# Optimization experiments

Hardware: AMD Instinct MI355X
Metric: run time of the kernel (lower is better)

## Reference

```python
import jax, jax.numpy as jnp
import numpy as np
import math

EPS = 1e-12
ANCHOR_T = 2.91  # anchor ratio threshold
G = 0.5          # grid-cell offset bias
OFF = np.array([[0, 0], [1, 0], [0, 1], [-1, 0], [0, -1]], dtype=np.float32) * G


def _bce_with_logits(x, t, pos_weight):
    # mean of -[pw*t*log(sig(x)) + (1-t)*log(1-sig(x))], numerically stable
    return jnp.mean((1.0 - t) * x + (1.0 + (pos_weight - 1.0) * t) * jax.nn.softplus(-x))


def _bbox_ciou(box1, box2):
    # box1, box2: [M,4] in xywh format (matches bbox_iou(x1y1x2y2=False, CIoU=True))
    b1_x1 = box1[:, 0] - box1[:, 2] / 2
    b1_x2 = box1[:, 0] + box1[:, 2] / 2 + EPS
    b1_y1 = box1[:, 1] - box1[:, 3] / 2
    b1_y2 = box1[:, 1] + box1[:, 3] / 2 + EPS
    b2_x1 = box2[:, 0] - box2[:, 2] / 2
    b2_x2 = box2[:, 0] + box2[:, 2] / 2 + EPS
    b2_y1 = box2[:, 1] - box2[:, 3] / 2
    b2_y2 = box2[:, 1] + box2[:, 3] / 2 + EPS
    inter = (jnp.clip(jnp.minimum(b1_x2, b2_x2) - jnp.maximum(b1_x1, b2_x1), 0)
             * jnp.clip(jnp.minimum(b1_y2, b2_y2) - jnp.maximum(b1_y1, b2_y1), 0))
    w1, h1 = b1_x2 - b1_x1, b1_y2 - b1_y1
    w2, h2 = b2_x2 - b2_x1, b2_y2 - b2_y1
    union = w1 * h1 + w2 * h2 - inter
    iou = inter / union
    cw = jnp.maximum(b1_x2, b2_x2) - jnp.minimum(b1_x1, b2_x1)
    ch = jnp.maximum(b1_y2, b2_y2) - jnp.minimum(b1_y1, b2_y1)
    c2 = cw ** 2 + ch ** 2
    rho2 = ((b2_x1 + b2_x2 - (b1_x1 + b1_x2)) ** 2 / 4
            + (b2_y1 + b2_y2 - (b1_y1 + b1_y2)) ** 2 / 4)
    v = (4.0 / math.pi ** 2) * (jnp.arctan(w2 / h2) - jnp.arctan(w1 / h1)) ** 2
    alpha = jax.lax.stop_gradient(v / (1.0 + EPS - iou + v))
    return iou - (rho2 / c2 + v * alpha)


def build_targets(p_shapes, targets, anchors):
    # Eager (non-jit) target assignment; returns per-level (tcls, tbox, indices, anch)
    na = anchors.shape[1]
    nl = anchors.shape[0]
    nt = targets.shape[0]
    ai = jnp.tile(jnp.arange(na, dtype=targets.dtype)[:, None], (1, nt))
    t7 = jnp.concatenate([jnp.tile(targets[None], (na, 1, 1)), ai[:, :, None]], axis=2)  # [na,nt,7]
    off = jnp.asarray(OFF)
    out = []
    for i in range(nl):
        anc = anchors[i]  # [na,2] in grid units
        W, H = p_shapes[i][3], p_shapes[i][2]
        gain = jnp.array([1, 1, W, H, W, H, 1], dtype=targets.dtype)
        t = t7 * gain
        r = t[:, :, 4:6] / anc[:, None, :]
        jmask = jnp.max(jnp.maximum(r, 1.0 / r), axis=2) < ANCHOR_T  # [na,nt]
        t = t[jmask]  # [M,7]
        gxy = t[:, 2:4]
        gxi = jnp.array([W, H], dtype=t.dtype) - gxy
        jk = (gxy % 1.0 < G) & (gxy > 1.0)
        lm = (gxi % 1.0 < G) & (gxi > 1.0)
        m5 = jnp.stack([jnp.ones_like(jk[:, 0]), jk[:, 0], jk[:, 1], lm[:, 0], lm[:, 1]])  # [5,M]
        t5 = jnp.tile(t[None], (5, 1, 1))[m5]
        offs = (jnp.zeros_like(gxy)[None] + off[:, None, :])[m5]
        b = t5[:, 0].astype(jnp.int32)
        c = t5[:, 1].astype(jnp.int32)
        gxy = t5[:, 2:4]
        gwh = t5[:, 4:6]
        gij = (gxy - offs).astype(jnp.int32)  # trunc == floor for positive coords
        gi, gj = gij[:, 0], gij[:, 1]
        a = t5[:, 6].astype(jnp.int32)
        tbox = jnp.concatenate([gxy - gij.astype(gxy.dtype), gwh], axis=1)
        out.append((c, tbox, (b, a, gj, gi), anc[a]))
    return out


def loss_from_built(p_list, built, num_classes):
    h_cls_pw, h_obj_pw = 0.631, 0.911
    h_giou, h_obj, h_cls = 0.0296, 0.301, 0.243
    balance = [4.0, 1.0, 0.4]
    lbox = jnp.zeros((), p_list[0].dtype)
    lobj = jnp.zeros((), p_list[0].dtype)
    lcls = jnp.zeros((), p_list[0].dtype)
    for i, pi in enumerate(p_list):
        tcls_i, tbox_i, (b, a, gj, gi), anch_i = built[i]
        tobj = jnp.zeros(pi.shape[:4], pi.dtype)
        n = b.shape[0]
        if n:
            ps = pi[b, a, gj, gi]  # [n, 5+nc]
            pxy = jax.nn.sigmoid(ps[:, :2]) * 2.0 - 0.5
            pwh = (jax.nn.sigmoid(ps[:, 2:4]) * 2.0) ** 2 * anch_i
            pbox = jnp.concatenate([pxy, pwh], axis=1)
            ciou = _bbox_ciou(pbox, tbox_i)
            lbox = lbox + jnp.mean(1.0 - ciou)
            tobj = tobj.at[b, a, gj, gi].set(
                jax.lax.stop_gradient(jnp.clip(ciou, 0.0, None)).astype(tobj.dtype))
            if num_classes > 1:
                tcl = jnp.zeros((n, num_classes), pi.dtype).at[jnp.arange(n), tcls_i].set(1.0)
                lcls = lcls + _bce_with_logits(ps[:, 5:], tcl, h_cls_pw)
        lobj = lobj + _bce_with_logits(pi[..., 4], tobj, h_obj_pw) * balance[i]
    s = 3.0 / len(p_list)
    lbox = lbox * h_giou * s
    lobj = lobj * h_obj * s
    lcls = lcls * h_cls * s
    loss = lbox + lobj + lcls
    bs = p_list[0].shape[0]
    return loss * bs, jnp.stack([lbox, lobj, lcls, loss])


def setup_inputs() -> dict:
    key = jax.random.key(0)
    k0, k1, k2, k3, k4, k5, k6 = jax.random.split(key, 7)
    B, nc, nt = 16, 80, 400
    p0 = jax.random.normal(k0, (B, 3, 80, 80, 5 + nc), jnp.float32)
    p1 = jax.random.normal(k1, (B, 3, 40, 40, 5 + nc), jnp.float32)
    p2 = jax.random.normal(k2, (B, 3, 20, 20, 5 + nc), jnp.float32)
    img = jax.random.randint(k3, (nt, 1), 0, B).astype(jnp.float32)
    cls = jax.random.randint(k4, (nt, 1), 0, nc).astype(jnp.float32)
    xy = jax.random.uniform(k5, (nt, 2), jnp.float32, 0.05, 0.95)
    wh = jax.random.uniform(k6, (nt, 2), jnp.float32, 0.02, 0.30)
    targets = jnp.concatenate([img, cls, xy, wh], axis=1)  # [nt,6]
    anchors = jnp.array([  # COCO yolov5 anchors / stride, [nl, na, 2]
        [[1.25, 1.625], [2.0, 3.75], [4.125, 2.875]],
        [[1.875, 3.8125], [3.875, 2.8125], [3.6875, 7.4375]],
        [[3.625, 2.8125], [4.875, 6.1875], [11.65625, 10.1875]]], dtype=jnp.float32)
    return {"p0": p0, "p1": p1, "p2": p2, "targets": targets, "anchors": anchors}


def reference(p0, p1, p2, targets, anchors):
    p_list = [p0, p1, p2]
    built = build_targets([p.shape for p in p_list], targets, anchors)
    return loss_from_built(p_list, built, num_classes=80)
```

## Files before the change

### kernel.cpp

```cpp
#include <hip/hip_runtime.h>
#include <math.h>

namespace {

constexpr int kMaxNT = 1024;
constexpr int kCells0 = 16 * 3 * 80 * 80;
constexpr int kCells1 = 16 * 3 * 40 * 40;
constexpr int kCells2 = 16 * 3 * 20 * 20;
constexpr int kCellsTotal = kCells0 + kCells1 + kCells2;

constexpr int kSlotsPerBlock = 16;
constexpr int kObjBlocks = 256;
constexpr int kObjThreads = kObjBlocks * 256;
constexpr int kObjIters = (kCellsTotal + kObjThreads - 1) / kObjThreads;

constexpr int kBPLMax = (15 * kMaxNT + kSlotsPerBlock - 1) / kSlotsPerBlock;

constexpr size_t kEbOff    = 0;
constexpr size_t kOpartOff = kEbOff + 4 * (3 * kBPLMax);

__device__ __forceinline__ float softplus_neg(float x) {
  return fmaxf(-x, 0.0f) + log1pf(expf(-fabsf(x)));
}

__global__ __launch_bounds__(256) void main_kernel(
    const float* __restrict__ p0, const float* __restrict__ p1,
    const float* __restrict__ p2, const float* __restrict__ targets,
    const float* __restrict__ anchors,
    float* __restrict__ eb_lbox, float* __restrict__ eb_lcls,
    float* __restrict__ eb_cnt, float* __restrict__ eb_ocorr,
    float* __restrict__ opart, int nt, int bpl) {
  int bid = blockIdx.x;
  int tid = threadIdx.x;
  int group = tid >> 6;
  int lane = tid & 63;

  if (bid < kObjBlocks) {
    int flat0 = bid * 256 + tid;
    float x[kObjIters];
#pragma unroll
    for (int j = 0; j < kObjIters; ++j) {
      int cell = flat0 + j * kObjThreads;
      float v = 0.0f;
      if (cell < kCellsTotal) {
        const float* p;
        int rel;
        if (cell < kCells0) { p = p0; rel = cell; }
        else if (cell < kCells0 + kCells1) { p = p1; rel = cell - kCells0; }
        else { p = p2; rel = cell - kCells0 - kCells1; }
        v = __builtin_nontemporal_load(&p[(size_t)rel * 85 + 4]);
      }
      x[j] = v;
    }
    float a0 = 0.f, a1 = 0.f, a2 = 0.f;
#pragma unroll
    for (int j = 0; j < kObjIters; ++j) {
      int cell = flat0 + j * kObjThreads;
      if (cell < kCellsTotal) {
        float v = x[j] + softplus_neg(x[j]);
        if (cell < kCells0) a0 += v;
        else if (cell < kCells0 + kCells1) a1 += v;
        else a2 += v;
      }
    }
    for (int o = 32; o > 0; o >>= 1) {
      a0 += __shfl_xor(a0, o);
      a1 += __shfl_xor(a1, o);
      a2 += __shfl_xor(a2, o);
    }
    __shared__ float s0[4], s1[4], s2[4];
    if (lane == 0) { s0[group] = a0; s1[group] = a1; s2[group] = a2; }
    __syncthreads();
    if (tid == 0) {
      opart[bid * 3 + 0] = s0[0] + s0[1] + s0[2] + s0[3];
      opart[bid * 3 + 1] = s1[0] + s1[1] + s1[2] + s1[3];
      opart[bid * 3 + 2] = s2[0] + s2[1] + s2[2] + s2[3];
    }
    return;
  }

  int ebid = bid - kObjBlocks;
  int level = ebid / bpl;
  int blk = ebid - level * bpl;
  int nslots = 15 * nt;
  int Wi = (level == 0) ? 80 : (level == 1) ? 40 : 20;
  float W = (float)Wi;
  const float* p = (level == 0) ? p0 : (level == 1) ? p1 : p2;

  float lbox_acc = 0.0f, cnt_acc = 0.0f, cls_acc = 0.0f, oc_acc = 0.0f;

  for (int k = 0; k < 4; ++k) {
    int s = blk * kSlotsPerBlock + group * 4 + k;
    if (s >= nslots) break;
    int r = s % 5;
    int pair = s / 5;
    int a = pair / nt;
    int ti = pair - a * nt;
    const float* tg = targets + ti * 6;
    float gx = tg[2] * W, gy = tg[3] * W;
    float gw = tg[4] * W, gh = tg[5] * W;
    float aw = anchors[(level * 3 + a) * 2 + 0];
    float ah = anchors[(level * 3 + a) * 2 + 1];
    float rw = gw / aw, rh = gh / ah;
    float m = fmaxf(fmaxf(rw, 1.0f / rw), fmaxf(rh, 1.0f / rh));
    bool pass = m < 2.91f;

    bool rowok = true;
    float ox = 0.0f, oy = 0.0f;
    if (r == 1)      { rowok = (fmodf(gx, 1.0f) < 0.5f) && (gx > 1.0f); ox = 0.5f; }
    else if (r == 2) { rowok = (fmodf(gy, 1.0f) < 0.5f) && (gy > 1.0f); oy = 0.5f; }
    else if (r == 3) { float gxi = W - gx;
                       rowok = (fmodf(gxi, 1.0f) < 0.5f) && (gxi > 1.0f); ox = -0.5f; }
    else if (r == 4) { float gyi = W - gy;
                       rowok = (fmodf(gyi, 1.0f) < 0.5f) && (gyi > 1.0f); oy = -0.5f; }

    if (!(pass && rowok)) continue;

    int gi = min(max((int)(gx - ox), 0), Wi - 1);
    int gj = min(max((int)(gy - oy), 0), Wi - 1);
    int b = (int)tg[0];
    int cls = (int)tg[1];
    int cell = ((b * 3 + a) * Wi + gj) * Wi + gi;
    const float* ps = p + (size_t)cell * 85;
    float tbx = gx - (float)gi, tby = gy - (float)gj;

    float px = 2.0f / (1.0f + expf(-ps[0])) - 0.5f;
    float py = 2.0f / (1.0f + expf(-ps[1])) - 0.5f;
    float sw = 2.0f / (1.0f + expf(-ps[2]));
    float sh = 2.0f / (1.0f + expf(-ps[3]));
    float pw = sw * sw * aw;
    float ph = sh * sh * ah;

    const float EPS = 1e-12f;
    float b1x1 = px - pw * 0.5f, b1x2 = px + pw * 0.5f + EPS;
    float b1y1 = py - ph * 0.5f, b1y2 = py + ph * 0.5f + EPS;
    float b2x1 = tbx - gw * 0.5f, b2x2 = tbx + gw * 0.5f + EPS;
    float b2y1 = tby - gh * 0.5f, b2y2 = tby + gh * 0.5f + EPS;
    float iw = fminf(b1x2, b2x2) - fmaxf(b1x1, b2x1);
    float ih = fminf(b1y2, b2y2) - fmaxf(b1y1, b2y1);
    float inter = fmaxf(iw, 0.0f) * fmaxf(ih, 0.0f);
    float w1 = b1x2 - b1x1, h1 = b1y2 - b1y1;
    float w2 = b2x2 - b2x1, h2 = b2y2 - b2y1;
    float uni = w1 * h1 + w2 * h2 - inter;
    float iou = inter / uni;
    float cwd = fmaxf(b1x2, b2x2) - fminf(b1x1, b2x1);
    float chd = fmaxf(b1y2, b2y2) - fminf(b1y1, b2y1);
    float c2 = cwd * cwd + chd * chd;
    float dx = (b2x1 + b2x2) - (b1x1 + b1x2);
    float dy = (b2y1 + b2y2) - (b1y1 + b1y2);
    float rho2 = dx * dx * 0.25f + dy * dy * 0.25f;
    float dat = atanf(w2 / h2) - atanf(w1 / h1);
    float v = 0.4052847345693511f * dat * dat;
    float alpha = v / (1.0f + EPS - iou + v);
    float ciou = iou - (rho2 / c2 + v * alpha);

    {
      float x = ps[5 + lane];
      float sp = softplus_neg(x);
      cls_acc += (lane == cls) ? (0.631f * sp) : (x + sp);
    }
    if (lane < 16) {
      int c = lane + 64;
      float x = ps[5 + c];
      float sp = softplus_neg(x);
      cls_acc += (c == cls) ? (0.631f * sp) : (x + sp);
    }

    float t = fmaxf(ciou, 0.0f);
    float xo = ps[4];
    oc_acc += t * (-xo - 0.089f * softplus_neg(xo));

    lbox_acc += 1.0f - ciou;
    cnt_acc += 1.0f;
  }

  for (int o = 32; o > 0; o >>= 1) cls_acc += __shfl_xor(cls_acc, o);

  __shared__ float sb[4], sc[4], sn[4], so[4];
  if (lane == 0) {
    sb[group] = lbox_acc; sc[group] = cls_acc;
    sn[group] = cnt_acc;  so[group] = oc_acc;
  }
  __syncthreads();
  if (tid == 0) {
    eb_lbox[ebid]  = sb[0] + sb[1] + sb[2] + sb[3];
    eb_lcls[ebid]  = sc[0] + sc[1] + sc[2] + sc[3];
    eb_cnt[ebid]   = sn[0] + sn[1] + sn[2] + sn[3];
    eb_ocorr[ebid] = so[0] + so[1] + so[2] + so[3];
  }
}

__global__ __launch_bounds__(256) void final_kernel(
    const float* __restrict__ eb_lbox, const float* __restrict__ eb_lcls,
    const float* __restrict__ eb_cnt, const float* __restrict__ eb_ocorr,
    const float* __restrict__ opart, float* __restrict__ out, int bpl) {
  int tid = threadIdx.x;
  int lane = tid & 63, w = tid >> 6;

  double vals[12];
#pragma unroll
  for (int k = 0; k < 12; ++k) vals[k] = 0.0;

#pragma unroll
  for (int lvl = 0; lvl < 3; ++lvl) {
    for (int j = tid; j < bpl; j += 256) {
      int bi = lvl * bpl + j;
      vals[lvl]     += (double)eb_lbox[bi];
      vals[3 + lvl] += (double)eb_lcls[bi];
      vals[6 + lvl] += (double)eb_cnt[bi];
      vals[9 + lvl] += (double)eb_ocorr[bi];
    }
  }
  for (int j = tid; j < kObjBlocks; j += 256) {
    vals[9]  += (double)opart[j * 3 + 0];
    vals[10] += (double)opart[j * 3 + 1];
    vals[11] += (double)opart[j * 3 + 2];
  }

  __shared__ double red[4][12];
#pragma unroll
  for (int k = 0; k < 12; ++k) {
    double v = vals[k];
    for (int o = 32; o > 0; o >>= 1) v += __shfl_xor(v, o);
    if (lane == 0) red[w][k] = v;
  }
  __syncthreads();
  if (tid == 0) {
    const double bal[3] = {4.0, 1.0, 0.4};
    const double ncl[3] = {(double)kCells0, (double)kCells1, (double)kCells2};
    double lbox = 0.0, lcls = 0.0, lobj = 0.0;
#pragma unroll
    for (int l = 0; l < 3; ++l) {
      double sB = red[0][l] + red[1][l] + red[2][l] + red[3][l];
      double sC = red[0][3 + l] + red[1][3 + l] + red[2][3 + l] + red[3][3 + l];
      double n  = red[0][6 + l] + red[1][6 + l] + red[2][6 + l] + red[3][6 + l];
      double sO = red[0][9 + l] + red[1][9 + l] + red[2][9 + l] + red[3][9 + l];
      if (n > 0.0) {
        lbox += sB / n;
        lcls += sC / (n * 80.0);
      }
      lobj += sO / ncl[l] * bal[l];
    }
    lbox *= 0.0296;
    lobj *= 0.301;
    lcls *= 0.243;
    double loss = lbox + lobj + lcls;
    out[0] = (float)(loss * 16.0);
    out[1] = (float)lbox;
    out[2] = (float)lobj;
    out[3] = (float)lcls;
    out[4] = (float)loss;
  }
}

}

extern "C" void kernel_launch(void* const* d_in, const int* in_sizes, int n_in,
                              void* d_out, int out_size, void* d_ws, size_t ws_size,
                              hipStream_t stream) {
  const float* p0 = (const float*)d_in[0];
  const float* p1 = (const float*)d_in[1];
  const float* p2 = (const float*)d_in[2];
  const float* targets = (const float*)d_in[3];
  const float* anchors = (const float*)d_in[4];
  int nt = in_sizes[3] / 6;
  if (nt > kMaxNT) nt = kMaxNT;
  int nslots = 15 * nt;
  int bpl = (nslots + kSlotsPerBlock - 1) / kSlotsPerBlock;

  float* wsf = (float*)d_ws;
  float* eb_lbox = wsf + kEbOff;
  float* eb_lcls = eb_lbox + 3 * kBPLMax;
  float* eb_cnt = eb_lcls + 3 * kBPLMax;
  float* eb_ocorr = eb_cnt + 3 * kBPLMax;
  float* opart = wsf + kOpartOff;

  int gridA = kObjBlocks + 3 * bpl;
  main_kernel<<<gridA, 256, 0, stream>>>(p0, p1, p2, targets, anchors,
                                         eb_lbox, eb_lcls, eb_cnt, eb_ocorr,
                                         opart, nt, bpl);
  final_kernel<<<1, 256, 0, stream>>>(eb_lbox, eb_lcls, eb_cnt, eb_ocorr, opart,
                                      (float*)d_out, bpl);
}
```

Measured before the change: 31.56 us.

## Replace final reduction kernel with atomics and last-block finalize

Per-block partial sums now go straight into a 12-float global accumulator with float atomicAdd, and a completion counter lets the last block compute the final loss. This drops the separate final reduction kernel and its partial-sum arrays. A tiny arm kernel is launched first to zero the accumulator and counter, so the launch count stays at two. The final sums change from a double-precision tree reduction to float atomics, which adds contention on a few addresses and makes the rounding order nondeterministic.

```diff
diff --git a/kernel.cpp b/kernel.cpp
--- a/kernel.cpp
+++ b/kernel.cpp
@@ -14,26 +14,28 @@
 constexpr int kObjThreads = kObjBlocks * 256;
 constexpr int kObjIters = (kCellsTotal + kObjThreads - 1) / kObjThreads;
 
-constexpr int kBPLMax = (15 * kMaxNT + kSlotsPerBlock - 1) / kSlotsPerBlock;
-
-constexpr size_t kEbOff    = 0;
-constexpr size_t kOpartOff = kEbOff + 4 * (3 * kBPLMax);
-
 __device__ __forceinline__ float softplus_neg(float x) {
   return fmaxf(-x, 0.0f) + log1pf(expf(-fabsf(x)));
+}
+
+__global__ void arm_kernel(float* __restrict__ acc, int* __restrict__ counter) {
+  int t = threadIdx.x;
+  if (t < 12) acc[t] = 0.0f;
+  if (t == 12) *counter = 0;
 }
 
 __global__ __launch_bounds__(256) void main_kernel(
     const float* __restrict__ p0, const float* __restrict__ p1,
     const float* __restrict__ p2, const float* __restrict__ targets,
     const float* __restrict__ anchors,
-    float* __restrict__ eb_lbox, float* __restrict__ eb_lcls,
-    float* __restrict__ eb_cnt, float* __restrict__ eb_ocorr,
-    float* __restrict__ opart, int nt, int bpl) {
+    float* __restrict__ acc, int* __restrict__ counter,
+    float* __restrict__ out, int nt, int bpl) {
   int bid = blockIdx.x;
   int tid = threadIdx.x;
   int group = tid >> 6;
   int lane = tid & 63;
+
+  __shared__ float s0[4], s1[4], s2[4], s3[4];
 
   if (bid < kObjBlocks) {
     int flat0 = bid * 256 + tid;
@@ -68,162 +70,144 @@
       a1 += __shfl_xor(a1, o);
       a2 += __shfl_xor(a2, o);
     }
-    __shared__ float s0[4], s1[4], s2[4];
     if (lane == 0) { s0[group] = a0; s1[group] = a1; s2[group] = a2; }
     __syncthreads();
     if (tid == 0) {
-      opart[bid * 3 + 0] = s0[0] + s0[1] + s0[2] + s0[3];
-      opart[bid * 3 + 1] = s1[0] + s1[1] + s1[2] + s1[3];
-      opart[bid * 3 + 2] = s2[0] + s2[1] + s2[2] + s2[3];
-    }
-    return;
+      float t0 = s0[0] + s0[1] + s0[2] + s0[3];
+      float t1 = s1[0] + s1[1] + s1[2] + s1[3];
+      float t2 = s2[0] + s2[1] + s2[2] + s2[3];
+      atomicAdd(&acc[9], t0);
+      atomicAdd(&acc[10], t1);
+      atomicAdd(&acc[11], t2);
+    }
+  } else {
+    int ebid = bid - kObjBlocks;
+    int level = ebid / bpl;
+    int blk = ebid - level * bpl;
+    int nslots = 15 * nt;
+    int Wi = (level == 0) ? 80 : (level == 1) ? 40 : 20;
+    float W = (float)Wi;
+    const float* p = (level == 0) ? p0 : (level == 1) ? p1 : p2;
+
+    float lbox_acc = 0.0f, cnt_acc = 0.0f, cls_acc = 0.0f, oc_acc = 0.0f;
+
+    for (int k = 0; k < 4; ++k) {
+      int s = blk * kSlotsPerBlock + group * 4 + k;
+      if (s >= nslots) break;
+      int r = s % 5;
+      int pair = s / 5;
+      int a = pair / nt;
+      int ti = pair - a * nt;
+      const float* tg = targets + ti * 6;
+      float gx = tg[2] * W, gy = tg[3] * W;
+      float gw = tg[4] * W, gh = tg[5] * W;
+      float aw = anchors[(level * 3 + a) * 2 + 0];
+      float ah = anchors[(level * 3 + a) * 2 + 1];
+      float rw = gw / aw, rh = gh / ah;
+      float m = fmaxf(fmaxf(rw, 1.0f / rw), fmaxf(rh, 1.0f / rh));
+      bool pass = m < 2.91f;
+
+      bool rowok = true;
+      float ox = 0.0f, oy = 0.0f;
+      if (r == 1)      { rowok = (fmodf(gx, 1.0f) < 0.5f) && (gx > 1.0f); ox = 0.5f; }
+      else if (r == 2) { rowok = (fmodf(gy, 1.0f) < 0.5f) && (gy > 1.0f); oy = 0.5f; }
+      else if (r == 3) { float gxi = W - gx;
+                         rowok = (fmodf(gxi, 1.0f) < 0.5f) && (gxi > 1.0f); ox = -0.5f; }
+      else if (r == 4) { float gyi = W - gy;
+                         rowok = (fmodf(gyi, 1.0f) < 0.5f) && (gyi > 1.0f); oy = -0.5f; }
+
+      if (!(pass && rowok)) continue;
+
+      int gi = min(max((int)(gx - ox), 0), Wi - 1);
+      int gj = min(max((int)(gy - oy), 0), Wi - 1);
+      int b = (int)tg[0];
+      int cls = (int)tg[1];
+      int cell = ((b * 3 + a) * Wi + gj) * Wi + gi;
+      const float* ps = p + (size_t)cell * 85;
+      float tbx = gx - (float)gi, tby = gy - (float)gj;
+
+      float px = 2.0f / (1.0f + expf(-ps[0])) - 0.5f;
+      float py = 2.0f / (1.0f + expf(-ps[1])) - 0.5f;
+      float sw = 2.0f / (1.0f + expf(-ps[2]));
+      float sh = 2.0f / (1.0f + expf(-ps[3]));
+      float pw = sw * sw * aw;
+      float ph = sh * sh * ah;
+
+      const float EPS = 1e-12f;
+      float b1x1 = px - pw * 0.5f, b1x2 = px + pw * 0.5f + EPS;
+      float b1y1 = py - ph * 0.5f, b1y2 = py + ph * 0.5f + EPS;
+      float b2x1 = tbx - gw * 0.5f, b2x2 = tbx + gw * 0.5f + EPS;
+      float b2y1 = tby - gh * 0.5f, b2y2 = tby + gh * 0.5f + EPS;
+      float iw = fminf(b1x2, b2x2) - fmaxf(b1x1, b2x1);
+      float ih = fminf(b1y2, b2y2) - fmaxf(b1y1, b2y1);
+      float inter = fmaxf(iw, 0.0f) * fmaxf(ih, 0.0f);
+      float w1 = b1x2 - b1x1, h1 = b1y2 - b1y1;
+      float w2 = b2x2 - b2x1, h2 = b2y2 - b2y1;
+      float uni = w1 * h1 + w2 * h2 - inter;
+      float iou = inter / uni;
+      float cwd = fmaxf(b1x2, b2x2) - fminf(b1x1, b2x1);
+      float chd = fmaxf(b1y2, b2y2) - fminf(b1y1, b2y1);
+      float c2 = cwd * cwd + chd * chd;
+      float dx = (b2x1 + b2x2) - (b1x1 + b1x2);
+      float dy = (b2y1 + b2y2) - (b1y1 + b1y2);
+      float rho2 = dx * dx * 0.25f + dy * dy * 0.25f;
+      float dat = atanf(w2 / h2) - atanf(w1 / h1);
+      float v = 0.4052847345693511f * dat * dat;
+      float alpha = v / (1.0f + EPS - iou + v);
+      float ciou = iou - (rho2 / c2 + v * alpha);
+
+      {
+        float x = ps[5 + lane];
+        float sp = softplus_neg(x);
+        cls_acc += (lane == cls) ? (0.631f * sp) : (x + sp);
+      }
+      if (lane < 16) {
+        int c = lane + 64;
+        float x = ps[5 + c];
+        float sp = softplus_neg(x);
+        cls_acc += (c == cls) ? (0.631f * sp) : (x + sp);
+      }
+
+      float t = fmaxf(ciou, 0.0f);
+      float xo = ps[4];
+      oc_acc += t * (-xo - 0.089f * softplus_neg(xo));
+
+      lbox_acc += 1.0f - ciou;
+      cnt_acc += 1.0f;
+    }
+
+    for (int o = 32; o > 0; o >>= 1) cls_acc += __shfl_xor(cls_acc, o);
+
+    if (lane == 0) {
+      s0[group] = lbox_acc; s1[group] = cls_acc;
+      s2[group] = cnt_acc;  s3[group] = oc_acc;
+    }
+    __syncthreads();
+    if (tid == 0) {
+      float tb = s0[0] + s0[1] + s0[2] + s0[3];
+      float tc = s1[0] + s1[1] + s1[2] + s1[3];
+      float tn = s2[0] + s2[1] + s2[2] + s2[3];
+      float to = s3[0] + s3[1] + s3[2] + s3[3];
+      if (tn != 0.0f) {
+        atomicAdd(&acc[0 + level], tb);
+        atomicAdd(&acc[3 + level], tc);
+        atomicAdd(&acc[6 + level], tn);
+        atomicAdd(&acc[9 + level], to);
+      }
+    }
   }
 
-  int ebid = bid - kObjBlocks;
-  int level = ebid / bpl;
-  int blk = ebid - level * bpl;
-  int nslots = 15 * nt;
-  int Wi = (level == 0) ? 80 : (level == 1) ? 40 : 20;
-  float W = (float)Wi;
-  const float* p = (level == 0) ? p0 : (level == 1) ? p1 : p2;
-
-  float lbox_acc = 0.0f, cnt_acc = 0.0f, cls_acc = 0.0f, oc_acc = 0.0f;
-
-  for (int k = 0; k < 4; ++k) {
-    int s = blk * kSlotsPerBlock + group * 4 + k;
-    if (s >= nslots) break;
-    int r = s % 5;
-    int pair = s / 5;
-    int a = pair / nt;
-    int ti = pair - a * nt;
-    const float* tg = targets + ti * 6;
-    float gx = tg[2] * W, gy = tg[3] * W;
-    float gw = tg[4] * W, gh = tg[5] * W;
-    float aw = anchors[(level * 3 + a) * 2 + 0];
-    float ah = anchors[(level * 3 + a) * 2 + 1];
-    float rw = gw / aw, rh = gh / ah;
-    float m = fmaxf(fmaxf(rw, 1.0f / rw), fmaxf(rh, 1.0f / rh));
-    bool pass = m < 2.91f;
-
-    bool rowok = true;
-    float ox = 0.0f, oy = 0.0f;
-    if (r == 1)      { rowok = (fmodf(gx, 1.0f) < 0.5f) && (gx > 1.0f); ox = 0.5f; }
-    else if (r == 2) { rowok = (fmodf(gy, 1.0f) < 0.5f) && (gy > 1.0f); oy = 0.5f; }
-    else if (r == 3) { float gxi = W - gx;
-                       rowok = (fmodf(gxi, 1.0f) < 0.5f) && (gxi > 1.0f); ox = -0.5f; }
-    else if (r == 4) { float gyi = W - gy;
-                       rowok = (fmodf(gyi, 1.0f) < 0.5f) && (gyi > 1.0f); oy = -0.5f; }
-
-    if (!(pass && rowok)) continue;
-
-    int gi = min(max((int)(gx - ox), 0), Wi - 1);
-    int gj = min(max((int)(gy - oy), 0), Wi - 1);
-    int b = (int)tg[0];
-    int cls = (int)tg[1];
-    int cell = ((b * 3 + a) * Wi + gj) * Wi + gi;
-    const float* ps = p + (size_t)cell * 85;
-    float tbx = gx - (float)gi, tby = gy - (float)gj;
-
-    float px = 2.0f / (1.0f + expf(-ps[0])) - 0.5f;
-    float py = 2.0f / (1.0f + expf(-ps[1])) - 0.5f;
-    float sw = 2.0f / (1.0f + expf(-ps[2]));
-    float sh = 2.0f / (1.0f + expf(-ps[3]));
-    float pw = sw * sw * aw;
-    float ph = sh * sh * ah;
-
-    const float EPS = 1e-12f;
-    float b1x1 = px - pw * 0.5f, b1x2 = px + pw * 0.5f + EPS;
-    float b1y1 = py - ph * 0.5f, b1y2 = py + ph * 0.5f + EPS;
-    float b2x1 = tbx - gw * 0.5f, b2x2 = tbx + gw * 0.5f + EPS;
-    float b2y1 = tby - gh * 0.5f, b2y2 = tby + gh * 0.5f + EPS;
-    float iw = fminf(b1x2, b2x2) - fmaxf(b1x1, b2x1);
-    float ih = fminf(b1y2, b2y2) - fmaxf(b1y1, b2y1);
-    float inter = fmaxf(iw, 0.0f) * fmaxf(ih, 0.0f);
-    float w1 = b1x2 - b1x1, h1 = b1y2 - b1y1;
-    float w2 = b2x2 - b2x1, h2 = b2y2 - b2y1;
-    float uni = w1 * h1 + w2 * h2 - inter;
-    float iou = inter / uni;
-    float cwd = fmaxf(b1x2, b2x2) - fminf(b1x1, b2x1);
-    float chd = fmaxf(b1y2, b2y2) - fminf(b1y1, b2y1);
-    float c2 = cwd * cwd + chd * chd;
-    float dx = (b2x1 + b2x2) - (b1x1 + b1x2);
-    float dy = (b2y1 + b2y2) - (b1y1 + b1y2);
-    float rho2 = dx * dx * 0.25f + dy * dy * 0.25f;
-    float dat = atanf(w2 / h2) - atanf(w1 / h1);
-    float v = 0.4052847345693511f * dat * dat;
-    float alpha = v / (1.0f + EPS - iou + v);
-    float ciou = iou - (rho2 / c2 + v * alpha);
-
-    {
-      float x = ps[5 + lane];
-      float sp = softplus_neg(x);
-      cls_acc += (lane == cls) ? (0.631f * sp) : (x + sp);
-    }
-    if (lane < 16) {
-      int c = lane + 64;
-      float x = ps[5 + c];
-      float sp = softplus_neg(x);
-      cls_acc += (c == cls) ? (0.631f * sp) : (x + sp);
-    }
-
-    float t = fmaxf(ciou, 0.0f);
-    float xo = ps[4];
-    oc_acc += t * (-xo - 0.089f * softplus_neg(xo));
-
-    lbox_acc += 1.0f - ciou;
-    cnt_acc += 1.0f;
-  }
-
-  for (int o = 32; o > 0; o >>= 1) cls_acc += __shfl_xor(cls_acc, o);
-
-  __shared__ float sb[4], sc[4], sn[4], so[4];
-  if (lane == 0) {
-    sb[group] = lbox_acc; sc[group] = cls_acc;
-    sn[group] = cnt_acc;  so[group] = oc_acc;
+  __shared__ bool isLast;
+  __shared__ float fin[12];
+  if (tid == 0) {
+    asm volatile("s_waitcnt vmcnt(0)" ::: "memory");
+    int old = atomicAdd(counter, 1);
+    isLast = (old == (int)gridDim.x - 1);
   }
   __syncthreads();
-  if (tid == 0) {
-    eb_lbox[ebid]  = sb[0] + sb[1] + sb[2] + sb[3];
-    eb_lcls[ebid]  = sc[0] + sc[1] + sc[2] + sc[3];
-    eb_cnt[ebid]   = sn[0] + sn[1] + sn[2] + sn[3];
-    eb_ocorr[ebid] = so[0] + so[1] + so[2] + so[3];
-  }
-}
-
-__global__ __launch_bounds__(256) void final_kernel(
-    const float* __restrict__ eb_lbox, const float* __restrict__ eb_lcls,
-    const float* __restrict__ eb_cnt, const float* __restrict__ eb_ocorr,
-    const float* __restrict__ opart, float* __restrict__ out, int bpl) {
-  int tid = threadIdx.x;
-  int lane = tid & 63, w = tid >> 6;
-
-  double vals[12];
-#pragma unroll
-  for (int k = 0; k < 12; ++k) vals[k] = 0.0;
-
-#pragma unroll
-  for (int lvl = 0; lvl < 3; ++lvl) {
-    for (int j = tid; j < bpl; j += 256) {
-      int bi = lvl * bpl + j;
-      vals[lvl]     += (double)eb_lbox[bi];
-      vals[3 + lvl] += (double)eb_lcls[bi];
-      vals[6 + lvl] += (double)eb_cnt[bi];
-      vals[9 + lvl] += (double)eb_ocorr[bi];
-    }
-  }
-  for (int j = tid; j < kObjBlocks; j += 256) {
-    vals[9]  += (double)opart[j * 3 + 0];
-    vals[10] += (double)opart[j * 3 + 1];
-    vals[11] += (double)opart[j * 3 + 2];
-  }
-
-  __shared__ double red[4][12];
-#pragma unroll
-  for (int k = 0; k < 12; ++k) {
-    double v = vals[k];
-    for (int o = 32; o > 0; o >>= 1) v += __shfl_xor(v, o);
-    if (lane == 0) red[w][k] = v;
-  }
+  if (!isLast) return;
+
+  if (tid < 12) fin[tid] = atomicAdd(&acc[tid], 0.0f);
   __syncthreads();
   if (tid == 0) {
     const double bal[3] = {4.0, 1.0, 0.4};
@@ -231,15 +215,12 @@
     double lbox = 0.0, lcls = 0.0, lobj = 0.0;
 #pragma unroll
     for (int l = 0; l < 3; ++l) {
-      double sB = red[0][l] + red[1][l] + red[2][l] + red[3][l];
-      double sC = red[0][3 + l] + red[1][3 + l] + red[2][3 + l] + red[3][3 + l];
-      double n  = red[0][6 + l] + red[1][6 + l] + red[2][6 + l] + red[3][6 + l];
-      double sO = red[0][9 + l] + red[1][9 + l] + red[2][9 + l] + red[3][9 + l];
+      double n = (double)fin[6 + l];
       if (n > 0.0) {
-        lbox += sB / n;
-        lcls += sC / (n * 80.0);
-      }
-      lobj += sO / ncl[l] * bal[l];
+        lbox += (double)fin[0 + l] / n;
+        lcls += (double)fin[3 + l] / (n * 80.0);
+      }
+      lobj += (double)fin[9 + l] / ncl[l] * bal[l];
     }
     lbox *= 0.0296;
     lobj *= 0.301;
@@ -268,17 +249,11 @@
   int nslots = 15 * nt;
   int bpl = (nslots + kSlotsPerBlock - 1) / kSlotsPerBlock;
 
-  float* wsf = (float*)d_ws;
-  float* eb_lbox = wsf + kEbOff;
-  float* eb_lcls = eb_lbox + 3 * kBPLMax;
-  float* eb_cnt = eb_lcls + 3 * kBPLMax;
-  float* eb_ocorr = eb_cnt + 3 * kBPLMax;
-  float* opart = wsf + kOpartOff;
-
+  float* acc = (float*)d_ws;
+  int* counter = (int*)((float*)d_ws + 12);
+
+  arm_kernel<<<1, 64, 0, stream>>>(acc, counter);
   int gridA = kObjBlocks + 3 * bpl;
   main_kernel<<<gridA, 256, 0, stream>>>(p0, p1, p2, targets, anchors,
-                                         eb_lbox, eb_lcls, eb_cnt, eb_ocorr,
-                                         opart, nt, bpl);
-  final_kernel<<<1, 256, 0, stream>>>(eb_lbox, eb_lcls, eb_cnt, eb_ocorr, opart,
-                                      (float*)d_out, bpl);
-}
+                                         acc, counter, (float*)d_out, nt, bpl);
+}
```

New measurement: 80.66 us. 2.56x slower.
